# Kernel tuning notes

Measured on AMD Instinct MI355X. Metric: run time of the kernel, lower is better.

## Reference

```python
import jax, jax.numpy as jnp
import numpy as np

B, H, S, D = 2, 16, 2048, 64


def setup_inputs() -> dict:
    key = jax.random.key(0)
    k1, k2, k3, k4, k5, k6 = jax.random.split(key, 6)
    q = jax.random.normal(k1, (B, H, S, D), dtype=jnp.float32)
    k = jax.random.normal(k2, (B, H, S, D), dtype=jnp.float32)
    v = jax.random.normal(k3, (B, H, S, D), dtype=jnp.float32)
    mask = jax.random.randint(k4, (B, S), 0, 2).astype(bool)
    taus = jax.random.uniform(k5, (H,), dtype=jnp.float32)
    attn_bias = jax.random.uniform(k6, (B, S, S), dtype=jnp.float32)
    return {"q": q, "k": k, "v": v, "mask": mask, "taus": taus, "attn_bias": attn_bias}


def reference(q, k, v, mask, taus, attn_bias):
    d = q.shape[-1]
    # scaled dot-product scores [b,h,i,j]
    sim = jnp.einsum('bhid,bhjd->bhij', q, k) / (d ** 0.5)
    # key padding mask over j (torch masked_fill with -finfo.max)
    neg_max = jnp.asarray(-jnp.finfo(sim.dtype).max, dtype=sim.dtype)
    sim = jnp.where(mask[:, None, None, :], sim, neg_max)
    # per-head tau-scaled additive bias: [b,i,j] * [h] -> [b,i,j,h] -> [b,h,i,j]
    bias = jnp.transpose(taus * attn_bias[..., None], (0, 3, 1, 2))
    sim = sim - bias
    attn = jax.nn.softmax(sim.astype(jnp.float32), axis=-1).astype(sim.dtype)
    out = jnp.einsum('bhij,bhjd->bhid', attn, v)
    return out
```

## Files before the change

### kernel.cpp

```cpp
#include <hip/hip_runtime.h>
#include <hip/hip_bf16.h>

#define Bdim 2
#define Hdim 16
#define Sdim 2048
#define Ddim 64
#define KVB 64
#define NT (Sdim / KVB)
#define CBT 20
#define CBS (CBT * KVB)

typedef __attribute__((ext_vector_type(4)))  float    f32x4;
typedef __attribute__((ext_vector_type(16))) float    f32x16;
typedef __attribute__((ext_vector_type(4)))  unsigned u32x4;
typedef __attribute__((ext_vector_type(8)))  short    s16x8;

#define NEGM   (-1.0e30f)
#define M_INIT (-30000.0f)
#define QS     0.18033688011112042f
#define L2E    1.4426950408889634f
#define THR    11.5f

typedef __attribute__((address_space(1))) void gv_t;
typedef __attribute__((address_space(3))) void lv_t;


static __device__ __forceinline__ unsigned pk2(float lo, float hi) {
  float2 t; t.x = lo; t.y = hi;
  __hip_bfloat162 h = __float22bfloat162_rn(t);
  unsigned u; __builtin_memcpy(&u, &h, 4); return u;
}

static __device__ __forceinline__ void pl32swap(unsigned a, unsigned b,
                                                unsigned &x, unsigned &y) {
#if __has_builtin(__builtin_amdgcn_permlane32_swap)
  typedef unsigned uv2 __attribute__((ext_vector_type(2)));
  uv2 r = __builtin_amdgcn_permlane32_swap(a, b, false, false);
  x = r[0]; y = r[1];
#else
  unsigned pa = (unsigned)__shfl_xor((int)a, 32);
  unsigned pb = (unsigned)__shfl_xor((int)b, 32);
  bool hi = (threadIdx.x & 32) != 0;
  x = hi ? pb : a;
  y = hi ? b : pa;
#endif
}

static __device__ __forceinline__ float xhalf_max(float t) {
  unsigned x, y;
  pl32swap(__float_as_uint(t), __float_as_uint(t), x, y);
  return fmaxf(__uint_as_float(x), __uint_as_float(y));
}
static __device__ __forceinline__ float xhalf_sum(float t) {
  unsigned x, y;
  pl32swap(__float_as_uint(t), __float_as_uint(t), x, y);
  return __uint_as_float(x) + __uint_as_float(y);
}

__global__ void scan_kernel(const int* __restrict__ mask, int* __restrict__ kept,
                            float* __restrict__ cmneg, int* __restrict__ meta)
{
  const int b = blockIdx.x;
  const int tid = threadIdx.x;
  __shared__ int part[256];
  const int base = tid * 8;
  int f[8]; int cnt = 0;
#pragma unroll
  for (int i = 0; i < 8; ++i) { f[i] = mask[b * Sdim + base + i] != 0; cnt += f[i]; }
  part[tid] = cnt;
  __syncthreads();
  for (int d = 1; d < 256; d <<= 1) {
    int v = (tid >= d) ? part[tid - d] : 0;
    __syncthreads();
    part[tid] += v;
    __syncthreads();
  }
  const int total = part[255];
  int p = part[tid] - cnt;
#pragma unroll
  for (int i = 0; i < 8; ++i) if (f[i]) kept[b * Sdim + (p++)] = base + i;
#pragma unroll
  for (int i = 0; i < 8; ++i) {
    int jc = base + i;
    cmneg[b * Sdim + jc] = (jc < total) ? 0.0f : NEGM;
    if (jc >= total) kept[b * Sdim + jc] = 0;
  }
  if (tid == 0) {
    int ntb = (total + 63) >> 6;
    int nte = (ntb + 1) & ~1;
    if (nte < 2) nte = 2;
    if (nte > CBT) nte = CBT;
    meta[b * 2] = nte;
    meta[b * 2 + 1] = total;
  }
}

__global__ __launch_bounds__(256, 2)
void bcompact_kernel(const float* __restrict__ bias, const int* __restrict__ kept,
                     const int* __restrict__ meta, float* __restrict__ cbias)
{
  const int b = blockIdx.x >> 11;
  const int i = blockIdx.x & 2047;
  const int tid = threadIdx.x;
  __shared__ float row[Sdim];
  const float* src = bias + ((size_t)b * Sdim + (size_t)i) * Sdim;
  *(f32x4*)&row[tid * 8]     = *(const f32x4*)(src + tid * 8);
  *(f32x4*)&row[tid * 8 + 4] = *(const f32x4*)(src + tid * 8 + 4);
  const int total = meta[b * 2 + 1];
  const int nv    = meta[b * 2] * (KVB / 4);
  const int* kb = kept + b * Sdim;
  __syncthreads();
  float* dst = cbias + ((size_t)b * Sdim + (size_t)i) * CBS;
  for (int v = tid; v < nv; v += 256) {
    int jc0 = v * 4;
    f32x4 o;
#pragma unroll
    for (int u = 0; u < 4; ++u) {
      int jc = jc0 + u;
      o[u] = (jc < total) ? row[kb[jc]] : 0.0f;
    }
    *(f32x4*)(dst + jc0) = o;
  }
}

__global__ __launch_bounds__(256, 2)
void pack_kernel(const float* __restrict__ k, const float* __restrict__ v,
                 const int* __restrict__ kept, const int* __restrict__ meta,
                 unsigned short* __restrict__ kimg,
                 unsigned short* __restrict__ vimg)
{
  const int jt = blockIdx.x;
  const int bh = blockIdx.y;
  const int tid = threadIdx.x;
  const int b = bh >> 4;
  const int nte = meta[b * 2];
  if (jt >= nte) return;
  const int total = meta[b * 2 + 1];
  const int* kb = kept + b * Sdim;
  const size_t basebh = (size_t)bh * Sdim * Ddim;
  const int jbase = jt * KVB;

  unsigned short* kout = kimg + ((size_t)(bh * NT + jt)) * 4096;
#pragma unroll
  for (int cc = 0; cc < 2; ++cc) {
    int c = tid + cc * 256;
    int blk = c >> 6, l = c & 63;
    int sub = blk >> 2, kc = blk & 3;
    int j = 32 * sub + (l & 31), e0 = 16 * kc + 8 * (l >> 5);
    int jg = jbase + j;
    float sel = (jg < total) ? 1.0f : 0.0f;
    const float* src = k + basebh + (size_t)kb[jg] * Ddim + e0;
    f32x4 a = *(const f32x4*)src, b2 = *(const f32x4*)(src + 4);
    u32x4 t;
    t[0] = pk2(a[0] * sel, a[1] * sel);   t[1] = pk2(a[2] * sel, a[3] * sel);
    t[2] = pk2(b2[0] * sel, b2[1] * sel); t[3] = pk2(b2[2] * sel, b2[3] * sel);
    *(u32x4*)(kout + (size_t)c * 8) = t;
  }

  __shared__ float Vl[64 * 64];
  {
    int r = tid >> 2, c4 = (tid & 3) * 16;
    int jg = jbase + r;
    float sel = (jg < total) ? 1.0f : 0.0f;
    const float* src = v + basebh + (size_t)kb[jg] * Ddim + c4;
#pragma unroll
    for (int i = 0; i < 4; ++i) {
      f32x4 a = *(const f32x4*)(src + 4 * i);
      a[0] *= sel; a[1] *= sel; a[2] *= sel; a[3] *= sel;
      *(f32x4*)&Vl[r * 64 + c4 + 4 * i] = a;
    }
  }
  __syncthreads();
  unsigned short* vout = vimg + ((size_t)(bh * NT + jt)) * 4096;
#pragma unroll
  for (int cc = 0; cc < 2; ++cc) {
    int c = tid + cc * 256;
    int blk = c >> 6, l = c & 63;
    int dn = blk >> 2, jc = blk & 3;
    int d = 32 * dn + (l & 31), jl0 = 16 * jc + 8 * (l >> 5);
    u32x4 t;
#pragma unroll
    for (int p = 0; p < 4; ++p)
      t[p] = pk2(Vl[(jl0 + 2 * p) * 64 + d], Vl[(jl0 + 2 * p + 1) * 64 + d]);
    *(u32x4*)(vout + (size_t)c * 8) = t;
  }
}

__global__ __launch_bounds__(256, 2)
void attn_kernel(const float* __restrict__ q,
                 unsigned short* __restrict__ kimg,
                 unsigned short* __restrict__ vimg,
                 const float* __restrict__ cmneg,
                 const float* __restrict__ taus, const float* __restrict__ cbias,
                 const int* __restrict__ meta,
                 float* __restrict__ out)
{
  const int tid  = threadIdx.x;
  const int wave = tid >> 6;
  const int lane = tid & 63;
  const int h2   = lane >> 5;
  const int q5   = lane & 31;

  const int bh = blockIdx.y;
  const int b  = bh >> 4, h = bh & 15;
  const int iw = blockIdx.x * 128 + wave * 32;
  const int qr = iw + q5;

  const int nte = meta[b * 2];
  const int np  = nte >> 1;

  __shared__ __align__(16) unsigned short Kl[4][4096];
  __shared__ __align__(16) unsigned short Vt[4][4096];
  __shared__ __align__(16) float Mg[Sdim];

  const float ntau = -taus[h] * L2E;
  const size_t qkvbase = ((size_t)bh) * Sdim * Ddim;
  const float* biasb = cbias + ((size_t)b * Sdim + (size_t)qr) * CBS;
  const float* mnegb = cmneg + b * Sdim;

  s16x8 qf[4];
  {
    const float* qrow = q + qkvbase + (size_t)qr * Ddim + 8 * h2;
#pragma unroll
    for (int kc = 0; kc < 4; ++kc) {
      f32x4 a = *(const f32x4*)(qrow + 16 * kc);
      f32x4 c = *(const f32x4*)(qrow + 16 * kc + 4);
      u32x4 t;
      t[0] = pk2(a[0] * QS, a[1] * QS); t[1] = pk2(a[2] * QS, a[3] * QS);
      t[2] = pk2(c[0] * QS, c[1] * QS); t[3] = pk2(c[2] * QS, c[3] * QS);
      s16x8 f; __builtin_memcpy(&f, &t, 16); qf[kc] = f;
    }
  }

  {
    int i0 = tid * 8;
    f32x4 a = *(const f32x4*)(mnegb + i0);
    f32x4 c = *(const f32x4*)(mnegb + i0 + 4);
    *(f32x4*)&Mg[i0]     = a;
    *(f32x4*)&Mg[i0 + 4] = c;
  }
  __syncthreads();

  auto stage = [&](int jt, int buf) {
    size_t tb = ((size_t)(bh * NT + jt)) * 4096 + wave * 1024 + lane * 8;
    int lo = wave * 1024;
#pragma unroll
    for (int i = 0; i < 2; ++i) {
      __builtin_amdgcn_global_load_lds((gv_t*)(kimg + tb + i * 512),
                                       (lv_t*)&Kl[buf][lo + i * 512], 16, 0, 0);
      __builtin_amdgcn_global_load_lds((gv_t*)(vimg + tb + i * 512),
                                       (lv_t*)&Vt[buf][lo + i * 512], 16, 0, 0);
    }
  };

  auto ldbias = [&](int t, f32x4 (&bv)[2][4]) {
    const int j0 = t * KVB;
#pragma unroll
    for (int sub = 0; sub < 2; ++sub)
#pragma unroll
      for (int c = 0; c < 4; ++c)
        bv[sub][c] = *(const f32x4*)(biasb + j0 + 32 * sub + 8 * c + 4 * h2);
  };

  f32x16 O[2];
  O[0] = (f32x16)(0.0f); O[1] = (f32x16)(0.0f);
  float m = M_INIT, l = 0.0f;

  f32x4 bvA[2][4], bvB[2][4];

  ldbias(0, bvA);
  stage(0, 0);
  stage(1, 1);
  ldbias(1, bvB);

  auto body = [&](int t, f32x4 (&bv)[2][4]) {
    const int cb = t & 3;
    const int j0 = t * KVB;

    const unsigned short* kb = &Kl[cb][0];
    f32x16 acc[2];
    acc[0] = (f32x16)(0.0f); acc[1] = (f32x16)(0.0f);
    __builtin_amdgcn_s_setprio(1);
#pragma unroll
    for (int sub = 0; sub < 2; ++sub)
#pragma unroll
      for (int kc = 0; kc < 4; ++kc) {
        s16x8 kf = *(const s16x8*)(kb + (sub * 4 + kc) * 512 + lane * 8);
        acc[sub] = __builtin_amdgcn_mfma_f32_32x32x16_bf16(kf, qf[kc], acc[sub], 0, 0, 0);
      }
    __builtin_amdgcn_s_setprio(0);

    f32x4 addv[2][4];
#pragma unroll
    for (int sub = 0; sub < 2; ++sub)
#pragma unroll
      for (int c = 0; c < 4; ++c) {
        f32x4 mnv = *(const f32x4*)&Mg[j0 + 32 * sub + 8 * c + 4 * h2];
        addv[sub][c] = ntau * bv[sub][c] + mnv;
      }

    if (t + 2 < nte) ldbias(t + 2, bv);

    float s[32];
#pragma unroll
    for (int sub = 0; sub < 2; ++sub)
#pragma unroll
      for (int r = 0; r < 16; ++r)
        s[16 * sub + r] = acc[sub][r] + addv[sub][r >> 2][r & 3];

    float m8[8];
#pragma unroll
    for (int i = 0; i < 8; ++i)
      m8[i] = fmaxf(fmaxf(s[i], s[i + 8]), fmaxf(s[i + 16], s[i + 24]));
    float tmax = fmaxf(fmaxf(fmaxf(m8[0], m8[1]), fmaxf(m8[2], m8[3])),
                       fmaxf(fmaxf(m8[4], m8[5]), fmaxf(m8[6], m8[7])));
    tmax = xhalf_max(tmax);

    if (!__all(tmax <= m + THR)) {
      float mn2 = fmaxf(m, tmax);
      float a = __builtin_amdgcn_exp2f(m - mn2);
      m = mn2; l *= a;
      O[0] *= a; O[1] *= a;
    }

#pragma unroll
    for (int i = 0; i < 32; ++i) s[i] = __builtin_amdgcn_exp2f(s[i] - m);
    float a16[16];
#pragma unroll
    for (int i = 0; i < 16; ++i) a16[i] = s[i] + s[i + 16];
#pragma unroll
    for (int i = 0; i < 8; ++i) a16[i] += a16[i + 8];
#pragma unroll
    for (int i = 0; i < 4; ++i) a16[i] += a16[i + 4];
    float rs = (a16[0] + a16[1]) + (a16[2] + a16[3]);
    l += xhalf_sum(rs);

    s16x8 pa[4];
#pragma unroll
    for (int sub = 0; sub < 2; ++sub) {
      unsigned pr[8];
#pragma unroll
      for (int i = 0; i < 8; ++i)
        pr[i] = pk2(s[16 * sub + 2 * i], s[16 * sub + 2 * i + 1]);
#pragma unroll
      for (int jc2 = 0; jc2 < 2; ++jc2) {
        unsigned x0, y0, x1, y1;
        pl32swap(pr[4 * jc2 + 0], pr[4 * jc2 + 2], x0, y0);
        pl32swap(pr[4 * jc2 + 1], pr[4 * jc2 + 3], x1, y1);
        u32x4 t2; t2[0] = x0; t2[1] = x1; t2[2] = y0; t2[3] = y1;
        s16x8 f; __builtin_memcpy(&f, &t2, 16);
        pa[2 * sub + jc2] = f;
      }
    }

    const unsigned short* vb = &Vt[cb][0];
    __builtin_amdgcn_s_setprio(1);
#pragma unroll
    for (int jc = 0; jc < 4; ++jc)
#pragma unroll
      for (int dn = 0; dn < 2; ++dn) {
        s16x8 vf = *(const s16x8*)(vb + (dn * 4 + jc) * 512 + lane * 8);
        O[dn] = __builtin_amdgcn_mfma_f32_32x32x16_bf16(vf, pa[jc], O[dn], 0, 0, 0);
      }
    __builtin_amdgcn_s_setprio(0);
  };

  for (int p = 0; p < np; ++p) {
    const int t0 = 2 * p, t1 = 2 * p + 1;

    if (p == np - 1) asm volatile("s_waitcnt vmcnt(0)" ::: "memory");
    else             asm volatile("s_waitcnt vmcnt(16)" ::: "memory");
    __builtin_amdgcn_s_barrier();

    if (p + 1 < np) {
      stage(t0 + 2, (t0 + 2) & 3);
      stage(t1 + 2, (t1 + 2) & 3);
    }

    body(t0, bvA);
    body(t1, bvB);
  }

  const float inv = 1.0f / l;
  float* orow = out + qkvbase + (size_t)qr * Ddim;
#pragma unroll
  for (int dn = 0; dn < 2; ++dn)
#pragma unroll
    for (int c = 0; c < 4; ++c) {
      f32x4 o;
      o[0] = O[dn][4 * c + 0] * inv; o[1] = O[dn][4 * c + 1] * inv;
      o[2] = O[dn][4 * c + 2] * inv; o[3] = O[dn][4 * c + 3] * inv;
      *(f32x4*)(orow + 32 * dn + 8 * c + 4 * h2) = o;
    }
}

extern "C" void kernel_launch(void* const* d_in, const int* in_sizes, int n_in,
                              void* d_out, int out_size, void* d_ws, size_t ws_size,
                              hipStream_t stream) {
  const float* q    = (const float*)d_in[0];
  const float* k    = (const float*)d_in[1];
  const float* v    = (const float*)d_in[2];
  const int*   mask = (const int*)d_in[3];
  const float* taus = (const float*)d_in[4];
  const float* bias = (const float*)d_in[5];
  float* out = (float*)d_out;

  char* ws = (char*)d_ws;
  int*   kept  = (int*)ws;
  int*   meta  = (int*)(ws + 16384);
  float* cmneg = (float*)(ws + 16640);
  unsigned short* kimg = (unsigned short*)(ws + 33024);
  unsigned short* vimg = kimg + 4194304;
  float* cbias = (float*)(vimg + 4194304);

  scan_kernel<<<dim3(Bdim), dim3(256), 0, stream>>>(mask, kept, cmneg, meta);
  pack_kernel<<<dim3(CBT, Bdim * Hdim), dim3(256), 0, stream>>>(
      k, v, kept, meta, kimg, vimg);
  bcompact_kernel<<<dim3(Bdim * Sdim), dim3(256), 0, stream>>>(
      bias, kept, meta, cbias);
  attn_kernel<<<dim3(Sdim / 128, Bdim * Hdim), dim3(256), 0, stream>>>(
      q, kimg, vimg, cmneg, taus, cbias, meta, out);
}
```

Measured before the change: 79.41 us.

## Merge pack and bias-compaction kernels; remap attention blocks for XCD-local bias reuse

Combines the K/V packing kernel and the bias compaction kernel into one launch, with block index ranges selecting each role, so one kernel launch and its tail gap go away. The attention grid is remapped so that the 16 heads sharing the same batch and query block land on the same XCD under round-robin dispatch, which should improve L2 reuse of the compacted bias rows. The remap assumes the hardware assigns consecutive workgroups round-robin across 8 XCDs. The merged kernel shares one shared buffer between both roles.

```diff
diff --git a/kernel.cpp b/kernel.cpp
--- a/kernel.cpp
+++ b/kernel.cpp
@@ -9,6 +9,8 @@
 #define NT (Sdim / KVB)
 #define CBT 20
 #define CBS (CBT * KVB)
+#define NPACK (CBT * Bdim * Hdim)
+#define NBC   (Bdim * Sdim)
 
 typedef __attribute__((ext_vector_type(4)))  float    f32x4;
 typedef __attribute__((ext_vector_type(16))) float    f32x16;
@@ -96,93 +98,93 @@
 }
 
 __global__ __launch_bounds__(256, 2)
-void bcompact_kernel(const float* __restrict__ bias, const int* __restrict__ kept,
-                     const int* __restrict__ meta, float* __restrict__ cbias)
-{
-  const int b = blockIdx.x >> 11;
-  const int i = blockIdx.x & 2047;
-  const int tid = threadIdx.x;
-  __shared__ float row[Sdim];
-  const float* src = bias + ((size_t)b * Sdim + (size_t)i) * Sdim;
-  *(f32x4*)&row[tid * 8]     = *(const f32x4*)(src + tid * 8);
-  *(f32x4*)&row[tid * 8 + 4] = *(const f32x4*)(src + tid * 8 + 4);
-  const int total = meta[b * 2 + 1];
-  const int nv    = meta[b * 2] * (KVB / 4);
-  const int* kb = kept + b * Sdim;
-  __syncthreads();
-  float* dst = cbias + ((size_t)b * Sdim + (size_t)i) * CBS;
-  for (int v = tid; v < nv; v += 256) {
-    int jc0 = v * 4;
-    f32x4 o;
-#pragma unroll
-    for (int u = 0; u < 4; ++u) {
-      int jc = jc0 + u;
-      o[u] = (jc < total) ? row[kb[jc]] : 0.0f;
-    }
-    *(f32x4*)(dst + jc0) = o;
-  }
-}
-
-__global__ __launch_bounds__(256, 2)
-void pack_kernel(const float* __restrict__ k, const float* __restrict__ v,
+void prep_kernel(const float* __restrict__ k, const float* __restrict__ v,
+                 const float* __restrict__ bias,
                  const int* __restrict__ kept, const int* __restrict__ meta,
                  unsigned short* __restrict__ kimg,
-                 unsigned short* __restrict__ vimg)
+                 unsigned short* __restrict__ vimg,
+                 float* __restrict__ cbias)
 {
-  const int jt = blockIdx.x;
-  const int bh = blockIdx.y;
+  const int bid = blockIdx.x;
   const int tid = threadIdx.x;
-  const int b = bh >> 4;
-  const int nte = meta[b * 2];
-  if (jt >= nte) return;
-  const int total = meta[b * 2 + 1];
-  const int* kb = kept + b * Sdim;
-  const size_t basebh = (size_t)bh * Sdim * Ddim;
-  const int jbase = jt * KVB;
-
-  unsigned short* kout = kimg + ((size_t)(bh * NT + jt)) * 4096;
-#pragma unroll
-  for (int cc = 0; cc < 2; ++cc) {
-    int c = tid + cc * 256;
-    int blk = c >> 6, l = c & 63;
-    int sub = blk >> 2, kc = blk & 3;
-    int j = 32 * sub + (l & 31), e0 = 16 * kc + 8 * (l >> 5);
-    int jg = jbase + j;
-    float sel = (jg < total) ? 1.0f : 0.0f;
-    const float* src = k + basebh + (size_t)kb[jg] * Ddim + e0;
-    f32x4 a = *(const f32x4*)src, b2 = *(const f32x4*)(src + 4);
-    u32x4 t;
-    t[0] = pk2(a[0] * sel, a[1] * sel);   t[1] = pk2(a[2] * sel, a[3] * sel);
-    t[2] = pk2(b2[0] * sel, b2[1] * sel); t[3] = pk2(b2[2] * sel, b2[3] * sel);
-    *(u32x4*)(kout + (size_t)c * 8) = t;
-  }
-
-  __shared__ float Vl[64 * 64];
-  {
-    int r = tid >> 2, c4 = (tid & 3) * 16;
-    int jg = jbase + r;
-    float sel = (jg < total) ? 1.0f : 0.0f;
-    const float* src = v + basebh + (size_t)kb[jg] * Ddim + c4;
-#pragma unroll
-    for (int i = 0; i < 4; ++i) {
-      f32x4 a = *(const f32x4*)(src + 4 * i);
-      a[0] *= sel; a[1] *= sel; a[2] *= sel; a[3] *= sel;
-      *(f32x4*)&Vl[r * 64 + c4 + 4 * i] = a;
-    }
-  }
-  __syncthreads();
-  unsigned short* vout = vimg + ((size_t)(bh * NT + jt)) * 4096;
-#pragma unroll
-  for (int cc = 0; cc < 2; ++cc) {
-    int c = tid + cc * 256;
-    int blk = c >> 6, l = c & 63;
-    int dn = blk >> 2, jc = blk & 3;
-    int d = 32 * dn + (l & 31), jl0 = 16 * jc + 8 * (l >> 5);
-    u32x4 t;
-#pragma unroll
-    for (int p = 0; p < 4; ++p)
-      t[p] = pk2(Vl[(jl0 + 2 * p) * 64 + d], Vl[(jl0 + 2 * p + 1) * 64 + d]);
-    *(u32x4*)(vout + (size_t)c * 8) = t;
+  __shared__ __align__(16) float lbuf[64 * 64];
+
+  if (bid < NPACK) {
+    const int jt = bid % CBT;
+    const int bh = bid / CBT;
+    const int b = bh >> 4;
+    const int nte = meta[b * 2];
+    if (jt >= nte) return;
+    const int total = meta[b * 2 + 1];
+    const int* kb = kept + b * Sdim;
+    const size_t basebh = (size_t)bh * Sdim * Ddim;
+    const int jbase = jt * KVB;
+
+    unsigned short* kout = kimg + ((size_t)(bh * NT + jt)) * 4096;
+#pragma unroll
+    for (int cc = 0; cc < 2; ++cc) {
+      int c = tid + cc * 256;
+      int blk = c >> 6, l = c & 63;
+      int sub = blk >> 2, kc = blk & 3;
+      int j = 32 * sub + (l & 31), e0 = 16 * kc + 8 * (l >> 5);
+      int jg = jbase + j;
+      float sel = (jg < total) ? 1.0f : 0.0f;
+      const float* src = k + basebh + (size_t)kb[jg] * Ddim + e0;
+      f32x4 a = *(const f32x4*)src, b2 = *(const f32x4*)(src + 4);
+      u32x4 t;
+      t[0] = pk2(a[0] * sel, a[1] * sel);   t[1] = pk2(a[2] * sel, a[3] * sel);
+      t[2] = pk2(b2[0] * sel, b2[1] * sel); t[3] = pk2(b2[2] * sel, b2[3] * sel);
+      *(u32x4*)(kout + (size_t)c * 8) = t;
+    }
+
+    {
+      int r = tid >> 2, c4 = (tid & 3) * 16;
+      int jg = jbase + r;
+      float sel = (jg < total) ? 1.0f : 0.0f;
+      const float* src = v + basebh + (size_t)kb[jg] * Ddim + c4;
+#pragma unroll
+      for (int i = 0; i < 4; ++i) {
+        f32x4 a = *(const f32x4*)(src + 4 * i);
+        a[0] *= sel; a[1] *= sel; a[2] *= sel; a[3] *= sel;
+        *(f32x4*)&lbuf[r * 64 + c4 + 4 * i] = a;
+      }
+    }
+    __syncthreads();
+    unsigned short* vout = vimg + ((size_t)(bh * NT + jt)) * 4096;
+#pragma unroll
+    for (int cc = 0; cc < 2; ++cc) {
+      int c = tid + cc * 256;
+      int blk = c >> 6, l = c & 63;
+      int dn = blk >> 2, jc = blk & 3;
+      int d = 32 * dn + (l & 31), jl0 = 16 * jc + 8 * (l >> 5);
+      u32x4 t;
+#pragma unroll
+      for (int p = 0; p < 4; ++p)
+        t[p] = pk2(lbuf[(jl0 + 2 * p) * 64 + d], lbuf[(jl0 + 2 * p + 1) * 64 + d]);
+      *(u32x4*)(vout + (size_t)c * 8) = t;
+    }
+  } else {
+    const int bid2 = bid - NPACK;
+    const int b = bid2 >> 11;
+    const int i = bid2 & 2047;
+    const float* src = bias + ((size_t)b * Sdim + (size_t)i) * Sdim;
+    *(f32x4*)&lbuf[tid * 8]     = *(const f32x4*)(src + tid * 8);
+    *(f32x4*)&lbuf[tid * 8 + 4] = *(const f32x4*)(src + tid * 8 + 4);
+    const int total = meta[b * 2 + 1];
+    const int nv    = meta[b * 2] * (KVB / 4);
+    const int* kb = kept + b * Sdim;
+    __syncthreads();
+    float* dst = cbias + ((size_t)b * Sdim + (size_t)i) * CBS;
+    for (int vv = tid; vv < nv; vv += 256) {
+      int jc0 = vv * 4;
+      f32x4 o;
+#pragma unroll
+      for (int u = 0; u < 4; ++u) {
+        int jc = jc0 + u;
+        o[u] = (jc < total) ? lbuf[kb[jc]] : 0.0f;
+      }
+      *(f32x4*)(dst + jc0) = o;
+    }
   }
 }
 
@@ -201,9 +203,15 @@
   const int h2   = lane >> 5;
   const int q5   = lane & 31;
 
-  const int bh = blockIdx.y;
-  const int b  = bh >> 4, h = bh & 15;
-  const int iw = blockIdx.x * 128 + wave * 32;
+  const int lin  = blockIdx.y * 16 + blockIdx.x;
+  const int xcd  = lin & 7;
+  const int slot = lin >> 3;
+  const int grp  = xcd * 4 + (slot >> 4);
+  const int h    = slot & 15;
+  const int b    = grp >> 4;
+  const int qb   = grp & 15;
+  const int bh   = b * 16 + h;
+  const int iw = qb * 128 + wave * 32;
   const int qr = iw + q5;
 
   const int nte = meta[b * 2];
@@ -414,10 +422,8 @@
   float* cbias = (float*)(vimg + 4194304);
 
   scan_kernel<<<dim3(Bdim), dim3(256), 0, stream>>>(mask, kept, cmneg, meta);
-  pack_kernel<<<dim3(CBT, Bdim * Hdim), dim3(256), 0, stream>>>(
-      k, v, kept, meta, kimg, vimg);
-  bcompact_kernel<<<dim3(Bdim * Sdim), dim3(256), 0, stream>>>(
-      bias, kept, meta, cbias);
+  prep_kernel<<<dim3(NPACK + NBC), dim3(256), 0, stream>>>(
+      k, v, bias, kept, meta, kimg, vimg, cbias);
   attn_kernel<<<dim3(Sdim / 128, Bdim * Hdim), dim3(256), 0, stream>>>(
       q, kimg, vimg, cmneg, taus, cbias, meta, out);
 }
```

Measured after the change: 76.02 us. 1.04x faster.
